# Kernel tuning notes

Hardware: AMD Instinct MI355X
Metric: run time of the kernel (lower is better)

Reference implementation:

```python
import jax, jax.numpy as jnp
import numpy as np
from math import factorial

L_MAX = 3
RC = 5.0
N_BASIS = 8
N_MAX = 4
N_CH = 16
K = N_MAX * N_CH  # 64 combined (radial x element-channel) features per l
NU_SCALING = 1.0
MP_SCALING = 0.5
OVERALL_SCALING = 1.0


def _fact(n):
    return float(factorial(n))


def _clebsch(j1, m1, j2, m2, J, M):
    # Racah formula for complex-basis Clebsch-Gordan coefficients
    if m1 + m2 != M or J < abs(j1 - j2) or J > j1 + j2:
        return 0.0
    pref = ((2 * J + 1) * _fact(J + j1 - j2) * _fact(J - j1 + j2) * _fact(j1 + j2 - J) / _fact(j1 + j2 + J + 1)) ** 0.5
    pref *= (_fact(J + M) * _fact(J - M) * _fact(j1 - m1) * _fact(j1 + m1) * _fact(j2 - m2) * _fact(j2 + m2)) ** 0.5
    s = 0.0
    for k in range(0, j1 + j2 - J + 1):
        d = [k, j1 + j2 - J - k, j1 - m1 - k, j2 + m2 - k, J - j2 + m1 + k, J - j1 - m2 + k]
        if min(d) < 0:
            continue
        den = 1.0
        for v in d:
            den *= _fact(v)
        s += (-1) ** k / den
    return pref * s


def _u_real(l):
    # complex -> real spherical-harmonic change of basis
    U = np.zeros((2 * l + 1, 2 * l + 1), dtype=complex)
    U[l, l] = 1.0
    for m in range(1, l + 1):
        U[l + m, l + m] = (-1) ** m / np.sqrt(2)
        U[l + m, l - m] = 1.0 / np.sqrt(2)
        U[l - m, l - m] = 1j / np.sqrt(2)
        U[l - m, l + m] = -1j * (-1) ** m / np.sqrt(2)
    return U


def _real_cg(l1, l2, L):
    Cc = np.zeros((2 * l1 + 1, 2 * l2 + 1, 2 * L + 1), dtype=complex)
    for m1 in range(-l1, l1 + 1):
        for m2 in range(-l2, l2 + 1):
            M = m1 + m2
            if abs(M) <= L:
                Cc[l1 + m1, l2 + m2, L + M] = _clebsch(l1, m1, l2, m2, L, M)
    T = np.einsum('am,bn,co,mno->abc', _u_real(l1), _u_real(l2), _u_real(L).conj(), Cc)
    re, im = T.real, T.imag
    out = re if np.abs(re).sum() >= np.abs(im).sum() else im
    return out.astype(np.float32)


CG = {}
for _l1 in range(L_MAX + 1):
    for _l2 in range(L_MAX + 1):
        for _L in range(abs(_l1 - _l2), min(_l1 + _l2, L_MAX) + 1):
            CG[(_l1, _l2, _L)] = jnp.asarray(_real_cg(_l1, _l2, _L))


def _spherical_harmonics(u):
    # real spherical harmonics up to l=3 on unit vectors, list of [E, 2l+1]
    x, y, z = u[:, 0], u[:, 1], u[:, 2]
    Y0 = 0.28209479177387814 * jnp.ones_like(x)[:, None]
    c1 = 0.4886025119029199
    Y1 = jnp.stack([c1 * y, c1 * z, c1 * x], axis=1)
    Y2 = jnp.stack([
        1.0925484305920792 * x * y,
        1.0925484305920792 * y * z,
        0.31539156525252005 * (3.0 * z * z - 1.0),
        1.0925484305920792 * x * z,
        0.5462742152960396 * (x * x - y * y),
    ], axis=1)
    Y3 = jnp.stack([
        0.5900435899266435 * y * (3.0 * x * x - y * y),
        2.890611442640554 * x * y * z,
        0.4570457994644658 * y * (5.0 * z * z - 1.0),
        0.3731763325901154 * z * (5.0 * z * z - 3.0),
        0.4570457994644658 * x * (5.0 * z * z - 1.0),
        1.445305721320277 * z * (x * x - y * y),
        0.5900435899266435 * x * (x * x - 3.0 * y * y),
    ], axis=1)
    return [Y0, Y1, Y2, Y3]


def _forward(positions, embeddings, W_inv, W_eq, W_mlp1, W_mlp2, w_last, species, senders, receivers):
    n_atoms = positions.shape[0]
    rij = positions[receivers] - positions[senders]            # [E,3]
    d = jnp.sqrt(jnp.sum(rij * rij, axis=1) + 1e-12)           # [E]
    u = rij / d[:, None]
    sh = [NU_SCALING * Y for Y in _spherical_harmonics(u)]
    fc = 0.5 * (jnp.cos(jnp.pi * d / RC) + 1.0) * (d < RC)     # smooth cutoff
    mu = jnp.asarray(np.linspace(0.0, RC, N_BASIS).astype(np.float32))
    sigma = RC / N_BASIS
    basis = jnp.exp(-0.5 * ((d[:, None] - mu) / sigma) ** 2) * fc[:, None]  # [E,B]
    emb = embeddings[species]                  # [N,C] center element embeddings
    emb_k = jnp.tile(emb, (1, N_MAX))          # [N,K]
    x_nb = emb[senders]                        # [E,C]
    # --- invariant message passing -> spherical expansion, list of [N, 2l+1, K]
    feats = []
    for l in range(L_MAX + 1):
        R = basis @ W_inv[l]                   # [E, N_MAX]
        msg = jnp.einsum('em,en,ec->emnc', sh[l], R, x_nb).reshape(-1, 2 * l + 1, K)
        feats.append(MP_SCALING * jax.ops.segment_sum(msg, receivers, num_segments=n_atoms))
    # --- generalized CG self-iteration (nu_max = 2 -> one iteration), residual
    new = []
    for L in range(L_MAX + 1):
        acc = feats[L]
        for l1 in range(L_MAX + 1):
            for l2 in range(L_MAX + 1):
                if (l1, l2, L) in CG:
                    acc = acc + jnp.einsum('nik,njk,ijm->nmk', feats[l1], feats[l2], CG[(l1, l2, L)])
        new.append(acc)
    feats = new
    # --- equivariant message passing layer (n_mp_layers = 2 -> one layer)
    embedded = [f * emb_k[:, None, :] for f in feats]
    nb = [f[senders] for f in embedded]        # gather sender features per l
    mp = []
    for L in range(L_MAX + 1):
        R = basis @ W_eq[L]                    # [E,K] learned radial weights
        acc = jnp.zeros((n_atoms, 2 * L + 1, K), dtype=positions.dtype)
        for l1 in range(L_MAX + 1):
            for l2 in range(L_MAX + 1):
                if (l1, l2, L) in CG:
                    m = jnp.einsum('ea,ebk,abM->eMk', sh[l1], nb[l2], CG[(l1, l2, L)])
                    acc = acc + jax.ops.segment_sum(m * R[:, None, :], receivers, num_segments=n_atoms)
        mp.append(MP_SCALING * acc)
    # --- final CG iterator requesting only L=0 invariants ('0_1')
    inv = mp[0][:, 0, :]
    for l in range(L_MAX + 1):
        inv = inv + jnp.einsum('nik,njk,ij->nk', mp[l], mp[l], CG[(l, l, 0)][:, :, 0])
    # --- invariant MLP + last layer, sum over atoms
    h = jax.nn.silu(inv @ W_mlp1)
    h = jax.nn.silu(h @ W_mlp2)
    e_atom = h @ w_last
    return (OVERALL_SCALING * jnp.sum(e_atom)).reshape(1)


def setup_inputs():
    key = jax.random.key(0)
    ks = jax.random.split(key, 10)
    N, E, NSPEC = 10000, 160000, 4
    return {
        'positions': jax.random.uniform(ks[0], (N, 3), dtype=jnp.float32) * 10.0,
        'embeddings': jax.random.normal(ks[4], (NSPEC, N_CH), dtype=jnp.float32),
        'W_inv': jax.random.normal(ks[5], (L_MAX + 1, N_BASIS, N_MAX), dtype=jnp.float32) / np.float32(np.sqrt(N_BASIS)),
        'W_eq': jax.random.normal(ks[6], (L_MAX + 1, N_BASIS, K), dtype=jnp.float32) / np.float32(np.sqrt(N_BASIS)),
        'W_mlp1': jax.random.normal(ks[7], (K, K), dtype=jnp.float32) / np.float32(np.sqrt(K)),
        'W_mlp2': jax.random.normal(ks[8], (K, K), dtype=jnp.float32) / np.float32(np.sqrt(K)),
        'w_last': jax.random.normal(ks[9], (K,), dtype=jnp.float32) / np.float32(np.sqrt(K)),
        'species': jax.random.randint(ks[1], (N,), 0, NSPEC),
        'senders': jax.random.randint(ks[2], (E,), 0, N),
        'receivers': jax.random.randint(ks[3], (E,), 0, N),
    }


def reference(positions, embeddings, W_inv, W_eq, W_mlp1, W_mlp2, w_last, species, senders, receivers):
    return _forward(positions, embeddings, W_inv, W_eq, W_mlp1, W_mlp2, w_last, species, senders, receivers)
```

## Files before the change

### kernel.cpp

```cpp
#include <hip/hip_runtime.h>
#include <math.h>

#define L_MAX 3
#define RCUT 5.0f
#define NB 8
#define NCH 16
#define KDIM 64
#define LMDIM 16
#define GSTRIDE 40

struct CD { double re; double im; };
struct UMat { CD m[7][7]; };
struct CGT { float v[7][7][7]; };

constexpr double cfact(int n){ double r=1.0; for(int i=2;i<=n;++i) r*=(double)i; return r; }
constexpr double cfabs(double x){ return x<0.0 ? -x : x; }
constexpr double csqrt_(double x){
  if (x<=0.0) return 0.0;
  double g = x>1.0 ? x : 1.0;
  for (int i=0;i<100;++i) g = 0.5*(g + x/g);
  return g;
}
constexpr double clebsch(int j1,int m1,int j2,int m2,int J,int M){
  if (m1+m2!=M) return 0.0;
  int ad = j1-j2; if (ad<0) ad=-ad;
  if (J<ad || J>j1+j2) return 0.0;
  double pref = csqrt_((2.0*J+1.0)*cfact(J+j1-j2)*cfact(J-j1+j2)*cfact(j1+j2-J)/cfact(j1+j2+J+1));
  pref *= csqrt_(cfact(J+M)*cfact(J-M)*cfact(j1-m1)*cfact(j1+m1)*cfact(j2-m2)*cfact(j2+m2));
  double s=0.0;
  for (int k=0;k<=j1+j2-J;++k){
    int d0=k,d1=j1+j2-J-k,d2=j1-m1-k,d3=j2+m2-k,d4=J-j2+m1+k,d5=J-j1-m2+k;
    if (d0<0||d1<0||d2<0||d3<0||d4<0||d5<0) continue;
    double den = cfact(d0)*cfact(d1)*cfact(d2)*cfact(d3)*cfact(d4)*cfact(d5);
    s += ((k&1)? -1.0:1.0)/den;
  }
  return pref*s;
}
constexpr UMat u_real(int l){
  UMat U{};
  U.m[l][l] = CD{1.0, 0.0};
  double is2 = csqrt_(0.5);
  for (int mm=1; mm<=l; ++mm){
    double sgn = (mm&1)? -1.0: 1.0;
    U.m[l+mm][l+mm] = CD{sgn*is2, 0.0};
    U.m[l+mm][l-mm] = CD{is2, 0.0};
    U.m[l-mm][l-mm] = CD{0.0, is2};
    U.m[l-mm][l+mm] = CD{0.0, -sgn*is2};
  }
  return U;
}
constexpr CGT real_cg(int l1,int l2,int L){
  double Cc[7][7][7] = {};
  for (int m1=-l1;m1<=l1;++m1)
    for (int m2=-l2;m2<=l2;++m2){
      int M=m1+m2;
      if (M>=-L && M<=L) Cc[l1+m1][l2+m2][L+M] = clebsch(l1,m1,l2,m2,L,M);
    }
  UMat U1=u_real(l1), U2=u_real(l2), U3=u_real(L);
  double Tre[7][7][7]={}, Tim[7][7][7]={};
  for (int a=0;a<2*l1+1;++a)
   for (int m=0;m<2*l1+1;++m){
     CD u1=U1.m[a][m];
     if (u1.re==0.0 && u1.im==0.0) continue;
     for (int b=0;b<2*l2+1;++b)
      for (int n=0;n<2*l2+1;++n){
        CD u2=U2.m[b][n];
        if (u2.re==0.0 && u2.im==0.0) continue;
        CD u12 = CD{u1.re*u2.re-u1.im*u2.im, u1.re*u2.im+u1.im*u2.re};
        for (int c=0;c<2*L+1;++c)
         for (int o=0;o<2*L+1;++o){
           CD u3=U3.m[c][o];
           if (u3.re==0.0 && u3.im==0.0) continue;
           double cc=Cc[m][n][o];
           if (cc==0.0) continue;
           double tr = u12.re*u3.re + u12.im*u3.im;
           double ti = u12.im*u3.re - u12.re*u3.im;
           Tre[a][b][c] += tr*cc;
           Tim[a][b][c] += ti*cc;
         }
      }
   }
  double sre=0.0, sim=0.0;
  for (int a=0;a<2*l1+1;++a) for (int b=0;b<2*l2+1;++b) for (int c=0;c<2*L+1;++c){
    sre += cfabs(Tre[a][b][c]); sim += cfabs(Tim[a][b][c]);
  }
  CGT out{};
  bool ure = (sre>=sim);
  for (int a=0;a<2*l1+1;++a) for (int b=0;b<2*l2+1;++b) for (int c=0;c<2*L+1;++c)
    out.v[a][b][c] = (float)(ure? Tre[a][b][c] : Tim[a][b][c]);
  return out;
}

struct alignas(64) CFlat { float v[256][16]; };
constexpr CFlat build_cflat(){
  CFlat o{};
  for (int l1=0;l1<=3;++l1)
   for (int l2=0;l2<=3;++l2){
     int lo = l1>l2 ? l1-l2 : l2-l1;
     int hi = (l1+l2<3)? l1+l2 : 3;
     for (int L=lo; L<=hi; ++L){
       CGT cg = real_cg(l1,l2,L);
       for (int i=0;i<2*l1+1;++i)
        for (int j=0;j<2*l2+1;++j)
         for (int m=0;m<2*L+1;++m){
           o.v[(L*L+m)*16 + (l2*l2+j)][l1*l1+i] += 0.5f*cg.v[i][j][m];
         }
     }
   }
  return o;
}
__device__ const CFlat CFLAT = build_cflat();

template<int l1,int l2,int L>
__device__ __forceinline__ void cg_contract(const float* __restrict__ f1,
                                            const float* __restrict__ f2,
                                            float* __restrict__ g){
  constexpr CGT cg = real_cg(l1,l2,L);
  #pragma unroll
  for (int i=0;i<2*l1+1;++i)
  #pragma unroll
  for (int j=0;j<2*l2+1;++j)
  #pragma unroll
  for (int m=0;m<2*L+1;++m){
    float c = cg.v[i][j][m];
    if (c != 0.0f) g[L*L+m] += c * f1[l1*l1+i] * f2[l2*l2+j];
  }
}

#define FOR_ALL_CG(X) \
  X(0,0,0) X(0,1,1) X(1,0,1) X(0,2,2) X(2,0,2) X(0,3,3) X(3,0,3) \
  X(1,1,0) X(1,1,1) X(1,1,2) \
  X(1,2,1) X(1,2,2) X(1,2,3) X(2,1,1) X(2,1,2) X(2,1,3) \
  X(1,3,2) X(1,3,3) X(3,1,2) X(3,1,3) \
  X(2,2,0) X(2,2,1) X(2,2,2) X(2,2,3) \
  X(2,3,1) X(2,3,2) X(2,3,3) X(3,2,1) X(3,2,2) X(3,2,3) \
  X(3,3,0) X(3,3,1) X(3,3,2) X(3,3,3)

__device__ __forceinline__ void all_contract(const float* __restrict__ f1,
                                             const float* __restrict__ f2,
                                             float* __restrict__ g){
#define XCG(a,b,c) cg_contract<a,b,c>(f1, f2, g);
  FOR_ALL_CG(XCG)
#undef XCG
}

__device__ __forceinline__ void compute_sh(float x, float y, float z, float* sh){
  sh[0]  = 0.28209479177387814f;
  sh[1]  = 0.4886025119029199f*y;
  sh[2]  = 0.4886025119029199f*z;
  sh[3]  = 0.4886025119029199f*x;
  sh[4]  = 1.0925484305920792f*x*y;
  sh[5]  = 1.0925484305920792f*y*z;
  sh[6]  = 0.31539156525252005f*(3.0f*z*z-1.0f);
  sh[7]  = 1.0925484305920792f*x*z;
  sh[8]  = 0.5462742152960396f*(x*x-y*y);
  sh[9]  = 0.5900435899266435f*y*(3.0f*x*x-y*y);
  sh[10] = 2.890611442640554f*x*y*z;
  sh[11] = 0.4570457994644658f*y*(5.0f*z*z-1.0f);
  sh[12] = 0.3731763325901154f*z*(5.0f*z*z-3.0f);
  sh[13] = 0.4570457994644658f*x*(5.0f*z*z-1.0f);
  sh[14] = 1.445305721320277f*z*(x*x-y*y);
  sh[15] = 0.5900435899266435f*x*(x*x-3.0f*y*y);
}

__global__ __launch_bounds__(256) void k_hist_d(
    const float* __restrict__ pos, const int* __restrict__ senders,
    const int* __restrict__ recv, int* __restrict__ counts, int E)
{
  int e = blockIdx.x*256 + threadIdx.x;
  if (e >= E) return;
  int s = senders[e], r = recv[e];
  float dx = pos[r*3+0]-pos[s*3+0];
  float dy = pos[r*3+1]-pos[s*3+1];
  float dz = pos[r*3+2]-pos[s*3+2];
  float d  = sqrtf(dx*dx+dy*dy+dz*dz + 1e-12f);
  if (d < RCUT) atomicAdd(&counts[r], 1);
}

__global__ __launch_bounds__(256) void k_scan1(const int* __restrict__ counts,
                                               int* __restrict__ offsets,
                                               int* __restrict__ bsum, int N){
  __shared__ int buf[256];
  int i = blockIdx.x*256 + threadIdx.x;
  int v = (i<N)? counts[i] : 0;
  buf[threadIdx.x] = v;
  __syncthreads();
  #pragma unroll
  for (int o=1;o<256;o<<=1){
    int t = (threadIdx.x>=o)? buf[threadIdx.x-o] : 0;
    __syncthreads();
    buf[threadIdx.x] += t;
    __syncthreads();
  }
  if (i<N) offsets[i] = buf[threadIdx.x] - v;
  if (threadIdx.x==255) bsum[blockIdx.x] = buf[255];
}

__global__ __launch_bounds__(256) void k_scan2(const int* __restrict__ bsum,
                                               int* __restrict__ bbase, int SB){
  __shared__ int buf[256];
  int v = (threadIdx.x<SB)? bsum[threadIdx.x] : 0;
  buf[threadIdx.x] = v;
  __syncthreads();
  #pragma unroll
  for (int o=1;o<256;o<<=1){
    int t = (threadIdx.x>=o)? buf[threadIdx.x-o] : 0;
    __syncthreads();
    buf[threadIdx.x] += t;
    __syncthreads();
  }
  if (threadIdx.x<SB) bbase[threadIdx.x] = buf[threadIdx.x] - v;
}

__global__ __launch_bounds__(256) void k_scan3(int* __restrict__ offsets,
                                               const int* __restrict__ bbase, int N){
  int i = blockIdx.x*256 + threadIdx.x;
  if (i<N) offsets[i] += bbase[blockIdx.x];
}

__global__ __launch_bounds__(256) void k_geom(
    const float* __restrict__ pos, const float* __restrict__ Winv,
    const int* __restrict__ species,
    const int* __restrict__ senders, const int* __restrict__ recv,
    const int* __restrict__ offsets, int* __restrict__ cursor,
    int* __restrict__ bucket_s, float* __restrict__ geomArr, int E)
{
  int e = blockIdx.x*256 + threadIdx.x;
  if (e >= E) return;
  int s = senders[e], r = recv[e];
  float dx = pos[r*3+0]-pos[s*3+0];
  float dy = pos[r*3+1]-pos[s*3+1];
  float dz = pos[r*3+2]-pos[s*3+2];
  float d  = sqrtf(dx*dx+dy*dy+dz*dz + 1e-12f);
  if (d >= RCUT) return;
  int p = atomicAdd(&cursor[r], 1);
  int slot = offsets[r] + p;
  float inv_d = 1.0f/d;
  float sh[16];
  compute_sh(dx*inv_d, dy*inv_d, dz*inv_d, sh);
  float fc = 0.5f*(cosf(d*(3.14159265358979323846f/RCUT))+1.0f);
  float b[8];
  #pragma unroll
  for (int q=0;q<NB;++q){
    float t = (d - (float)((double)q*(5.0/7.0))) * 1.6f;
    b[q] = expf(-0.5f*t*t)*fc;
  }
  float* g = geomArr + (size_t)slot*GSTRIDE;
  #pragma unroll
  for (int i=0;i<16;++i) g[i] = sh[i];
  #pragma unroll
  for (int q=0;q<8;++q) g[16+q] = b[q];
  #pragma unroll
  for (int l=0;l<4;++l)
    #pragma unroll
    for (int n=0;n<4;++n){
      float acc=0.0f;
      #pragma unroll
      for (int q=0;q<NB;++q) acc += b[q]*Winv[l*32+q*4+n];
      g[24+l*4+n] = acc;
    }
  bucket_s[slot] = s | (species[s]<<16);
}

__global__ __launch_bounds__(256) void kA_gather_tp(
    const float* __restrict__ emb, const int* __restrict__ species,
    const int* __restrict__ offsets, const int* __restrict__ counts,
    const int* __restrict__ bucket_s, const float* __restrict__ geomArr,
    float* __restrict__ feats, int N)
{
  int wv = threadIdx.x>>6;
  int r = blockIdx.x*4 + wv;
  if (r >= N) return;
  int lane = threadIdx.x & 63;
  int n = lane>>4, c = lane&15;
  int off = offsets[r], cnt = counts[r];
  float f[16];
  #pragma unroll
  for (int lm=0; lm<16; ++lm) f[lm]=0.0f;
  int pk = (cnt>0)? bucket_s[off] : 0;
  for (int j=0; j<cnt; ++j){
    int spec = pk>>16;
    if (j+1<cnt) pk = bucket_s[off+j+1];
    const float* gm = geomArr + (size_t)(off+j)*GSTRIDE;
    float e5 = 0.5f*emb[spec*NCH+c];
    float4 s0 = *(const float4*)(gm+0);
    float4 s1 = *(const float4*)(gm+4);
    float4 s2 = *(const float4*)(gm+8);
    float4 s3 = *(const float4*)(gm+12);
    float t0 = gm[24+0+n]*e5;
    float t1 = gm[24+4+n]*e5;
    float t2 = gm[24+8+n]*e5;
    float t3 = gm[24+12+n]*e5;
    f[0] += s0.x*t0;
    f[1] += s0.y*t1;  f[2] += s0.z*t1;  f[3] += s0.w*t1;
    f[4] += s1.x*t2;  f[5] += s1.y*t2;  f[6] += s1.z*t2;  f[7] += s1.w*t2;  f[8] += s2.x*t2;
    f[9] += s2.y*t3;  f[10]+= s2.z*t3;  f[11]+= s2.w*t3;
    f[12]+= s3.x*t3;  f[13]+= s3.y*t3;  f[14]+= s3.z*t3;  f[15]+= s3.w*t3;
  }
  float g[16];
  #pragma unroll
  for (int lm=0; lm<16; ++lm) g[lm]=f[lm];
  all_contract(f, f, g);
  float ek = emb[species[r]*NCH + c];
  float* fp = feats + (size_t)r*(LMDIM*KDIM) + lane;
  #pragma unroll
  for (int lm=0; lm<16; ++lm) fp[lm*KDIM] = g[lm]*ek;
}

template<int l>
__device__ __forceinline__ float inv_term(const float* m){
  constexpr CGT cg = real_cg(l,l,0);
  float a=0.0f;
  #pragma unroll
  for (int i=0;i<2*l+1;++i)
  #pragma unroll
  for (int j=0;j<2*l+1;++j){
    float c = cg.v[i][j][0];
    if (c != 0.0f) a += c*m[l*l+i]*m[l*l+j];
  }
  return a;
}

__global__ __launch_bounds__(256) void kB_mp2_mlp(
    const float* __restrict__ Weq,
    const float* __restrict__ W1, const float* __restrict__ W2,
    const float* __restrict__ wl,
    const int* __restrict__ offsets, const int* __restrict__ counts,
    const int* __restrict__ bucket_s, const float* __restrict__ geomArr,
    const float* __restrict__ embedded, float* __restrict__ eatom, int N)
{
  __shared__ __align__(16) float Ash[4][256];
  int wv = threadIdx.x>>6;
  int r = blockIdx.x*4 + wv;
  if (r >= N) return;
  int k = threadIdx.x & 63;
  int off = offsets[r], cnt = counts[r];
  float* Arow = Ash[wv];
  float m[16];
  #pragma unroll
  for (int i=0;i<16;++i) m[i]=0.0f;

  int pk = (cnt>0)? bucket_s[off] : 0;
  for (int j=0; j<cnt; ++j){
    int s = pk & 0xFFFF;
    if (j+1<cnt) pk = bucket_s[off+j+1];
    const float* npp = embedded + (size_t)s*(LMDIM*KDIM) + k;
    float nb[16];
    #pragma unroll
    for (int lm=0; lm<16; ++lm) nb[lm]=npp[lm*KDIM];
    const float* gm = geomArr + (size_t)(off+j)*GSTRIDE;
    float4 s0 = *(const float4*)(gm+0);
    float4 s1 = *(const float4*)(gm+4);
    float4 s2 = *(const float4*)(gm+8);
    float4 s3 = *(const float4*)(gm+12);
    float4 b0 = *(const float4*)(gm+16);
    float4 b1 = *(const float4*)(gm+20);
    float sh[16] = {s0.x,s0.y,s0.z,s0.w, s1.x,s1.y,s1.z,s1.w,
                    s2.x,s2.y,s2.z,s2.w, s3.x,s3.y,s3.z,s3.w};
    float b[8] = {b0.x,b0.y,b0.z,b0.w, b1.x,b1.y,b1.z,b1.w};
    float Req[4];
    #pragma unroll
    for (int L=0;L<4;++L){
      float acc=0.0f;
      #pragma unroll
      for (int q=0;q<NB;++q) acc += b[q]*Weq[L*(NB*KDIM) + q*KDIM + k];
      Req[L]=acc;
    }
    #pragma unroll
    for (int q=0;q<4;++q){
      int ent = q*64 + k;
      const float4* c4 = (const float4*)CFLAT.v[ent];
      float4 c0=c4[0], c1=c4[1], c2=c4[2], c3=c4[3];
      float acc = c0.x*sh[0]+c0.y*sh[1]+c0.z*sh[2]+c0.w*sh[3]
                + c1.x*sh[4]+c1.y*sh[5]+c1.z*sh[6]+c1.w*sh[7]
                + c2.x*sh[8]+c2.y*sh[9]+c2.z*sh[10]+c2.w*sh[11]
                + c3.x*sh[12]+c3.y*sh[13]+c3.z*sh[14]+c3.w*sh[15];
      Arow[ent] = acc;
    }
    #pragma unroll
    for (int M=0;M<16;++M){
      const int L = (M==0)?0 : (M<4)?1 : (M<9)?2 : 3;
      const float4* a4 = (const float4*)(Arow + M*16);
      float4 a0=a4[0], a1=a4[1], a2=a4[2], a3=a4[3];
      float acc = a0.x*nb[0]+a0.y*nb[1]+a0.z*nb[2]+a0.w*nb[3]
                + a1.x*nb[4]+a1.y*nb[5]+a1.z*nb[6]+a1.w*nb[7]
                + a2.x*nb[8]+a2.y*nb[9]+a2.z*nb[10]+a2.w*nb[11]
                + a3.x*nb[12]+a3.y*nb[13]+a3.z*nb[14]+a3.w*nb[15];
      m[M] += acc*Req[L];
    }
  }

  float inv = m[0];
  inv += inv_term<0>(m);
  inv += inv_term<1>(m);
  inv += inv_term<2>(m);
  inv += inv_term<3>(m);
  Arow[k] = inv;
  float a=0.0f;
  #pragma unroll
  for (int c=0;c<64;++c) a += Arow[c]*W1[c*64+k];
  a = a / (1.0f + expf(-a));
  Arow[64+k] = a;
  float h2=0.0f;
  #pragma unroll
  for (int c=0;c<64;++c) h2 += Arow[64+c]*W2[c*64+k];
  h2 = h2 / (1.0f + expf(-h2));
  float e = h2*wl[k];
  #pragma unroll
  for (int o=32; o>0; o>>=1) e += __shfl_down(e, o);
  if (k==0) eatom[r] = e;
}

__global__ __launch_bounds__(256) void k_reduce(const float* __restrict__ eatom,
                                                float* __restrict__ out, int N){
  __shared__ float buf[256];
  float a=0.0f;
  for (int i=threadIdx.x; i<N; i+=256) a += eatom[i];
  buf[threadIdx.x]=a;
  __syncthreads();
  #pragma unroll
  for (int o=128;o>0;o>>=1){
    if (threadIdx.x<o) buf[threadIdx.x]+=buf[threadIdx.x+o];
    __syncthreads();
  }
  if (threadIdx.x==0) out[0]=buf[0];
}

extern "C" void kernel_launch(void* const* d_in, const int* in_sizes, int n_in,
                              void* d_out, int out_size, void* d_ws, size_t ws_size,
                              hipStream_t stream)
{
  const float* pos     = (const float*)d_in[0];
  const float* emb     = (const float*)d_in[1];
  const float* Winv    = (const float*)d_in[2];
  const float* Weq     = (const float*)d_in[3];
  const float* W1      = (const float*)d_in[4];
  const float* W2      = (const float*)d_in[5];
  const float* wl      = (const float*)d_in[6];
  const int*   species = (const int*)d_in[7];
  const int*   senders = (const int*)d_in[8];
  const int*   recv    = (const int*)d_in[9];
  int N = in_sizes[7];
  int E = in_sizes[8];

  char* ws = (char*)d_ws;
  float* feats   = (float*)ws;
  float* geomArr = feats + (size_t)N*(LMDIM*KDIM);
  float* eatom   = geomArr + (size_t)E*GSTRIDE;
  int*   counts  = (int*)(eatom + N);
  int*   cursor  = counts + N;
  int*   offsets = cursor + N;
  int*   bsum    = offsets + N;
  int*   bbase   = bsum + 256;
  int*   bucket_s= bbase + 256;

  hipMemsetAsync(counts, 0, 2*(size_t)N*sizeof(int), stream);

  int ebl = (E+255)/256;
  int abl = (N+3)/4;
  int SB  = (N+255)/256;
  k_hist_d<<<ebl, 256, 0, stream>>>(pos, senders, recv, counts, E);
  k_scan1<<<SB, 256, 0, stream>>>(counts, offsets, bsum, N);
  k_scan2<<<1, 256, 0, stream>>>(bsum, bbase, SB);
  k_scan3<<<SB, 256, 0, stream>>>(offsets, bbase, N);
  k_geom<<<ebl, 256, 0, stream>>>(pos, Winv, species, senders, recv, offsets, cursor,
                                  bucket_s, geomArr, E);
  kA_gather_tp<<<abl, 256, 0, stream>>>(emb, species, offsets, counts, bucket_s, geomArr, feats, N);
  kB_mp2_mlp<<<abl, 256, 0, stream>>>(Weq, W1, W2, wl, offsets, counts, bucket_s, geomArr,
                                      feats, eatom, N);
  k_reduce<<<1, 256, 0, stream>>>(eatom, (float*)d_out, N);
}
```

Baseline: 245.6 us.

## Split each node's edge loop across four waves and symmetrize CG product

Both gather kernels now assign one block per receiver node, with its four waves striding over the node's edges and reducing partial sums through shared memory. This is meant to cut the serial per-node edge latency that one wave per node had before, at the cost of fewer nodes per block and a block-wide sync. In the tensor-product kernel the self-product CG contraction is rebuilt as a symmetrized upper-triangular table and its 16 output rows are split across the four waves, reducing redundant multiplies. The MLP tail runs on one wave only, leaving three waves idle there.

```diff
diff --git a/kernel.cpp b/kernel.cpp
--- a/kernel.cpp
+++ b/kernel.cpp
@@ -111,37 +111,56 @@
 }
 __device__ const CFlat CFLAT = build_cflat();
 
-template<int l1,int l2,int L>
-__device__ __forceinline__ void cg_contract(const float* __restrict__ f1,
-                                            const float* __restrict__ f2,
-                                            float* __restrict__ g){
-  constexpr CGT cg = real_cg(l1,l2,L);
-  #pragma unroll
-  for (int i=0;i<2*l1+1;++i)
-  #pragma unroll
-  for (int j=0;j<2*l2+1;++j)
-  #pragma unroll
-  for (int m=0;m<2*L+1;++m){
-    float c = cg.v[i][j][m];
-    if (c != 0.0f) g[L*L+m] += c * f1[l1*l1+i] * f2[l2*l2+j];
-  }
-}
-
-#define FOR_ALL_CG(X) \
-  X(0,0,0) X(0,1,1) X(1,0,1) X(0,2,2) X(2,0,2) X(0,3,3) X(3,0,3) \
-  X(1,1,0) X(1,1,1) X(1,1,2) \
-  X(1,2,1) X(1,2,2) X(1,2,3) X(2,1,1) X(2,1,2) X(2,1,3) \
-  X(1,3,2) X(1,3,3) X(3,1,2) X(3,1,3) \
-  X(2,2,0) X(2,2,1) X(2,2,2) X(2,2,3) \
-  X(2,3,1) X(2,3,2) X(2,3,3) X(3,2,1) X(3,2,2) X(3,2,3) \
-  X(3,3,0) X(3,3,1) X(3,3,2) X(3,3,3)
-
-__device__ __forceinline__ void all_contract(const float* __restrict__ f1,
-                                             const float* __restrict__ f2,
-                                             float* __restrict__ g){
-#define XCG(a,b,c) cg_contract<a,b,c>(f1, f2, g);
-  FOR_ALL_CG(XCG)
-#undef XCG
+struct CSym { float v[16][16][16]; };
+constexpr CSym build_csym(){
+  CSym o{};
+  for (int l1=0;l1<=3;++l1)
+   for (int l2=0;l2<=3;++l2){
+     int lo = l1>l2 ? l1-l2 : l2-l1;
+     int hi = (l1+l2<3)? l1+l2 : 3;
+     for (int L=lo; L<=hi; ++L){
+       CGT cg = real_cg(l1,l2,L);
+       for (int i=0;i<2*l1+1;++i)
+        for (int j=0;j<2*l2+1;++j)
+         for (int m=0;m<2*L+1;++m)
+           o.v[L*L+m][l1*l1+i][l2*l2+j] += cg.v[i][j][m];
+     }
+   }
+  for (int M=0;M<16;++M)
+   for (int i=0;i<16;++i)
+    for (int j=i+1;j<16;++j){
+      o.v[M][i][j] += o.v[M][j][i];
+      o.v[M][j][i] = 0.0f;
+    }
+  return o;
+}
+
+template<int M>
+__device__ __forceinline__ float tp_row(const float* __restrict__ f){
+  constexpr CSym CS = build_csym();
+  float g = 0.0f;
+  #pragma unroll
+  for (int i=0;i<16;++i)
+  #pragma unroll
+  for (int j=i;j<16;++j){
+    float c = CS.v[M][i][j];
+    if (c != 0.0f) g += c * f[i] * f[j];
+  }
+  return g;
+}
+
+template<int l>
+__device__ __forceinline__ float inv_term(const float* m){
+  constexpr CGT cg = real_cg(l,l,0);
+  float a=0.0f;
+  #pragma unroll
+  for (int i=0;i<2*l+1;++i)
+  #pragma unroll
+  for (int j=0;j<2*l+1;++j){
+    float c = cg.v[i][j][0];
+    if (c != 0.0f) a += c*m[l*l+i]*m[l*l+j];
+  }
+  return a;
 }
 
 __device__ __forceinline__ void compute_sh(float x, float y, float z, float* sh){
@@ -262,25 +281,23 @@
   bucket_s[slot] = s | (species[s]<<16);
 }
 
-__global__ __launch_bounds__(256) void kA_gather_tp(
+__global__ __launch_bounds__(256,4) void kA_gather_tp(
     const float* __restrict__ emb, const int* __restrict__ species,
     const int* __restrict__ offsets, const int* __restrict__ counts,
     const int* __restrict__ bucket_s, const float* __restrict__ geomArr,
     float* __restrict__ feats, int N)
 {
-  int wv = threadIdx.x>>6;
-  int r = blockIdx.x*4 + wv;
-  if (r >= N) return;
-  int lane = threadIdx.x & 63;
+  __shared__ float Msh[4][16][64];
+  int r = blockIdx.x;
+  int wv = threadIdx.x>>6, lane = threadIdx.x & 63;
   int n = lane>>4, c = lane&15;
   int off = offsets[r], cnt = counts[r];
   float f[16];
   #pragma unroll
   for (int lm=0; lm<16; ++lm) f[lm]=0.0f;
-  int pk = (cnt>0)? bucket_s[off] : 0;
-  for (int j=0; j<cnt; ++j){
+  for (int j=wv; j<cnt; j+=4){
+    int pk = bucket_s[off+j];
     int spec = pk>>16;
-    if (j+1<cnt) pk = bucket_s[off+j+1];
     const float* gm = geomArr + (size_t)(off+j)*GSTRIDE;
     float e5 = 0.5f*emb[spec*NCH+c];
     float4 s0 = *(const float4*)(gm+0);
@@ -297,31 +314,29 @@
     f[9] += s2.y*t3;  f[10]+= s2.z*t3;  f[11]+= s2.w*t3;
     f[12]+= s3.x*t3;  f[13]+= s3.y*t3;  f[14]+= s3.z*t3;  f[15]+= s3.w*t3;
   }
-  float g[16];
-  #pragma unroll
-  for (int lm=0; lm<16; ++lm) g[lm]=f[lm];
-  all_contract(f, f, g);
+  #pragma unroll
+  for (int i=0;i<16;++i) Msh[wv][i][lane] = f[i];
+  __syncthreads();
+  #pragma unroll
+  for (int i=0;i<16;++i)
+    f[i] = Msh[0][i][lane]+Msh[1][i][lane]+Msh[2][i][lane]+Msh[3][i][lane];
+  float g[4];
+  switch (wv){
+    case 0: g[0]=tp_row<0>(f);  g[1]=tp_row<1>(f);  g[2]=tp_row<2>(f);  g[3]=tp_row<3>(f);  break;
+    case 1: g[0]=tp_row<4>(f);  g[1]=tp_row<5>(f);  g[2]=tp_row<6>(f);  g[3]=tp_row<7>(f);  break;
+    case 2: g[0]=tp_row<8>(f);  g[1]=tp_row<9>(f);  g[2]=tp_row<10>(f); g[3]=tp_row<11>(f); break;
+    default:g[0]=tp_row<12>(f); g[1]=tp_row<13>(f); g[2]=tp_row<14>(f); g[3]=tp_row<15>(f); break;
+  }
   float ek = emb[species[r]*NCH + c];
   float* fp = feats + (size_t)r*(LMDIM*KDIM) + lane;
   #pragma unroll
-  for (int lm=0; lm<16; ++lm) fp[lm*KDIM] = g[lm]*ek;
-}
-
-template<int l>
-__device__ __forceinline__ float inv_term(const float* m){
-  constexpr CGT cg = real_cg(l,l,0);
-  float a=0.0f;
-  #pragma unroll
-  for (int i=0;i<2*l+1;++i)
-  #pragma unroll
-  for (int j=0;j<2*l+1;++j){
-    float c = cg.v[i][j][0];
-    if (c != 0.0f) a += c*m[l*l+i]*m[l*l+j];
-  }
-  return a;
-}
-
-__global__ __launch_bounds__(256) void kB_mp2_mlp(
+  for (int t=0;t<4;++t){
+    int M = wv*4+t;
+    fp[M*KDIM] = (f[M] + g[t])*ek;
+  }
+}
+
+__global__ __launch_bounds__(256,4) void kB_mp2_mlp(
     const float* __restrict__ Weq,
     const float* __restrict__ W1, const float* __restrict__ W2,
     const float* __restrict__ wl,
@@ -329,10 +344,10 @@
     const int* __restrict__ bucket_s, const float* __restrict__ geomArr,
     const float* __restrict__ embedded, float* __restrict__ eatom, int N)
 {
+  __shared__ float Msh[4][16][64];
   __shared__ __align__(16) float Ash[4][256];
+  int r = blockIdx.x;
   int wv = threadIdx.x>>6;
-  int r = blockIdx.x*4 + wv;
-  if (r >= N) return;
   int k = threadIdx.x & 63;
   int off = offsets[r], cnt = counts[r];
   float* Arow = Ash[wv];
@@ -340,10 +355,8 @@
   #pragma unroll
   for (int i=0;i<16;++i) m[i]=0.0f;
 
-  int pk = (cnt>0)? bucket_s[off] : 0;
-  for (int j=0; j<cnt; ++j){
-    int s = pk & 0xFFFF;
-    if (j+1<cnt) pk = bucket_s[off+j+1];
+  for (int j=wv; j<cnt; j+=4){
+    int s = bucket_s[off+j] & 0xFFFF;
     const float* npp = embedded + (size_t)s*(LMDIM*KDIM) + k;
     float nb[16];
     #pragma unroll
@@ -390,20 +403,30 @@
     }
   }
 
+  #pragma unroll
+  for (int i=0;i<16;++i) Msh[wv][i][k] = m[i];
+  __syncthreads();
+  if (wv != 0) return;
+
+  #pragma unroll
+  for (int i=0;i<16;++i)
+    m[i] = Msh[0][i][k]+Msh[1][i][k]+Msh[2][i][k]+Msh[3][i][k];
+
   float inv = m[0];
   inv += inv_term<0>(m);
   inv += inv_term<1>(m);
   inv += inv_term<2>(m);
   inv += inv_term<3>(m);
-  Arow[k] = inv;
+  float* B = Ash[0];
+  B[k] = inv;
   float a=0.0f;
   #pragma unroll
-  for (int c=0;c<64;++c) a += Arow[c]*W1[c*64+k];
+  for (int c=0;c<64;++c) a += B[c]*W1[c*64+k];
   a = a / (1.0f + expf(-a));
-  Arow[64+k] = a;
+  B[64+k] = a;
   float h2=0.0f;
   #pragma unroll
-  for (int c=0;c<64;++c) h2 += Arow[64+c]*W2[c*64+k];
+  for (int c=0;c<64;++c) h2 += B[64+c]*W2[c*64+k];
   h2 = h2 / (1.0f + expf(-h2));
   float e = h2*wl[k];
   #pragma unroll
@@ -457,7 +480,6 @@
   hipMemsetAsync(counts, 0, 2*(size_t)N*sizeof(int), stream);
 
   int ebl = (E+255)/256;
-  int abl = (N+3)/4;
   int SB  = (N+255)/256;
   k_hist_d<<<ebl, 256, 0, stream>>>(pos, senders, recv, counts, E);
   k_scan1<<<SB, 256, 0, stream>>>(counts, offsets, bsum, N);
@@ -465,8 +487,8 @@
   k_scan3<<<SB, 256, 0, stream>>>(offsets, bbase, N);
   k_geom<<<ebl, 256, 0, stream>>>(pos, Winv, species, senders, recv, offsets, cursor,
                                   bucket_s, geomArr, E);
-  kA_gather_tp<<<abl, 256, 0, stream>>>(emb, species, offsets, counts, bucket_s, geomArr, feats, N);
-  kB_mp2_mlp<<<abl, 256, 0, stream>>>(Weq, W1, W2, wl, offsets, counts, bucket_s, geomArr,
-                                      feats, eatom, N);
+  kA_gather_tp<<<N, 256, 0, stream>>>(emb, species, offsets, counts, bucket_s, geomArr, feats, N);
+  kB_mp2_mlp<<<N, 256, 0, stream>>>(Weq, W1, W2, wl, offsets, counts, bucket_s, geomArr,
+                                    feats, eatom, N);
   k_reduce<<<1, 256, 0, stream>>>(eatom, (float*)d_out, N);
 }
```

Measured after the change: 485.1 us. +97.5%, slower.
